# Kernel tuning notes

Hardware: AMD Instinct MI355X
Metric: run time of the kernel (lower is better)

Reference implementation:

```python
import jax, jax.numpy as jnp
import numpy as np

D_MODEL = 1024
N_HEADS = 16
D_HEAD = 64
SEQ = 2048
BATCH = 2
ATTN_SCALE = float(np.sqrt(D_HEAD))  # cfg.use_attn_scale = True
NEG_INF = -1e9


def setup_inputs() -> dict:
    key = jax.random.key(0)
    ks = jax.random.split(key, 8)
    s = 0.02
    return {
        "query_input": jax.random.normal(ks[0], (BATCH, SEQ, D_MODEL), jnp.float32),
        "key_input": jax.random.normal(ks[1], (BATCH, SEQ, D_MODEL), jnp.float32),
        "value_input": jax.random.normal(ks[2], (BATCH, SEQ, D_MODEL), jnp.float32),
        "W_Q": jax.random.normal(ks[3], (N_HEADS, D_MODEL, D_HEAD), jnp.float32) * s,
        "W_K": jax.random.normal(ks[4], (N_HEADS, D_MODEL, D_HEAD), jnp.float32) * s,
        "W_V": jax.random.normal(ks[5], (N_HEADS, D_MODEL, D_HEAD), jnp.float32) * s,
        "W_O": jax.random.normal(ks[6], (N_HEADS, D_HEAD, D_MODEL), jnp.float32) * s,
        "b_Q": jnp.zeros((N_HEADS, D_HEAD), jnp.float32),
        "b_K": jnp.zeros((N_HEADS, D_HEAD), jnp.float32),
        "b_V": jnp.zeros((N_HEADS, D_HEAD), jnp.float32),
        "b_O": jnp.zeros((D_MODEL,), jnp.float32),
    }


def reference(query_input, key_input, value_input, W_Q, W_K, W_V, W_O, b_Q, b_K, b_V, b_O):
    # QKV projections: [batch, pos, d_model] x [head, d_model, d_head] -> [batch, pos, head, d_head]
    q = jnp.einsum("bpd,hde->bphe", query_input, W_Q) + b_Q
    k = jnp.einsum("bpd,hde->bphe", key_input, W_K) + b_K
    v = jnp.einsum("bpd,hde->bphe", value_input, W_V) + b_V

    # attn scores [batch, head, query_pos, key_pos]
    scores = jnp.einsum("bqhe,bkhe->bhqk", q, k) / ATTN_SCALE

    # causal mask (attn_type == 'global'): tril over [n_ctx, n_ctx] sliced to seq
    causal = jnp.tril(jnp.ones((SEQ, SEQ), bool))
    scores = jnp.where(causal[None, None, :, :], scores, NEG_INF)

    pattern = jax.nn.softmax(scores, axis=-1)

    # z: [batch, query_pos, head, d_head]
    z = jnp.einsum("bhqk,bkhe->bqhe", pattern, v)

    # output projection: [batch, pos, d_model]
    out = jnp.einsum("bqhe,hed->bqd", z, W_O) + b_O
    return out
```

## Files before the change

kernel.cpp:

```cpp
#include <hip/hip_runtime.h>
#include <stdint.h>


typedef __attribute__((ext_vector_type(8))) short short8;
typedef __attribute__((ext_vector_type(4))) float floatx4;
typedef __attribute__((ext_vector_type(4))) unsigned int uintx4;

#define MFMA16(a, b, c) __builtin_amdgcn_mfma_f32_16x16x32_bf16(a, b, c, 0, 0, 0)

__device__ __forceinline__ unsigned short f2b(float f) {
  unsigned int u = __builtin_bit_cast(unsigned int, f);
  u = (u + 0x7fffu + ((u >> 16) & 1u)) >> 16;
  return (unsigned short)u;
}
__device__ __forceinline__ float exp2f_fast(float x) {
#if __has_builtin(__builtin_amdgcn_exp2f)
  return __builtin_amdgcn_exp2f(x);
#else
  return exp2f(x);
#endif
}
__device__ __forceinline__ unsigned int pack2_bf16(float lo, float hi) {
#if __has_builtin(__builtin_amdgcn_perm)
  return __builtin_amdgcn_perm(__builtin_bit_cast(unsigned int, hi),
                               __builtin_bit_cast(unsigned int, lo), 0x07060302u);
#else
  return (__builtin_bit_cast(unsigned int, lo) >> 16) |
         (__builtin_bit_cast(unsigned int, hi) & 0xffff0000u);
#endif
}

__device__ __forceinline__ void async_copy16(void* lds, const void* g) {
  __builtin_amdgcn_global_load_lds(
      (const __attribute__((address_space(1))) unsigned int*)g,
      (__attribute__((address_space(3))) unsigned int*)lds, 16, 0, 0);
}

__global__ __launch_bounds__(256) void conv_x3(const float* __restrict__ a,
                                               const float* __restrict__ b,
                                               const float* __restrict__ c,
                                               unsigned short* __restrict__ out) {
  const float* in = (blockIdx.y == 0) ? a : ((blockIdx.y == 1) ? b : c);
  size_t i = (size_t)blockIdx.x * 256 + threadIdx.x;
  float4 v = ((const float4*)in)[i];
  ushort4 u;
  u.x = f2b(v.x); u.y = f2b(v.y); u.z = f2b(v.z); u.w = f2b(v.w);
  ((ushort4*)(out + (size_t)blockIdx.y * 4194304))[i] = u;
}

__global__ __launch_bounds__(256) void conv_w3(const float* __restrict__ a,
                                               const float* __restrict__ b,
                                               const float* __restrict__ c,
                                               unsigned short* __restrict__ out) {
  __shared__ float T[64][65];
  const float* in = (blockIdx.y == 0) ? a : ((blockIdx.y == 1) ? b : c);
  const int t = threadIdx.x, rr = t >> 4, cc = t & 15;
  const int h = blockIdx.x >> 4, d0 = (blockIdx.x & 15) << 6;
#pragma unroll
  for (int it = 0; it < 4; ++it) {
    int dl = it * 16 + rr;
    float4 v = *(const float4*)&in[(size_t)h * 65536 + (size_t)(d0 + dl) * 64 + cc * 4];
    T[dl][cc * 4 + 0] = v.x; T[dl][cc * 4 + 1] = v.y;
    T[dl][cc * 4 + 2] = v.z; T[dl][cc * 4 + 3] = v.w;
  }
  __syncthreads();
  unsigned short* ob = out + (size_t)blockIdx.y * 1048576;
#pragma unroll
  for (int it = 0; it < 4; ++it) {
    int e = it * 16 + rr;
    ushort4 u;
    u.x = f2b(T[cc * 4 + 0][e]); u.y = f2b(T[cc * 4 + 1][e]);
    u.z = f2b(T[cc * 4 + 2][e]); u.w = f2b(T[cc * 4 + 3][e]);
    *(ushort4*)&ob[(size_t)(h * 64 + e) * 1024 + d0 + cc * 4] = u;
  }
}

__global__ __launch_bounds__(256) void conv_wo(const float* __restrict__ in,
                                               unsigned short* __restrict__ out) {
  __shared__ float T[64][65];
  const int t = threadIdx.x, rr = t >> 4, cc = t & 15;
  const int r0 = (blockIdx.x & 15) << 6;
  const int c0 = (blockIdx.x >> 4) << 6;
#pragma unroll
  for (int it = 0; it < 4; ++it) {
    int rl = it * 16 + rr;
    float4 v = *(const float4*)&in[(size_t)(r0 + rl) * 1024 + c0 + cc * 4];
    T[rl][cc * 4 + 0] = v.x; T[rl][cc * 4 + 1] = v.y;
    T[rl][cc * 4 + 2] = v.z; T[rl][cc * 4 + 3] = v.w;
  }
  __syncthreads();
#pragma unroll
  for (int it = 0; it < 4; ++it) {
    int dl = it * 16 + rr;
    ushort4 u;
    u.x = f2b(T[cc * 4 + 0][dl]); u.y = f2b(T[cc * 4 + 1][dl]);
    u.z = f2b(T[cc * 4 + 2][dl]); u.w = f2b(T[cc * 4 + 3][dl]);
    *(ushort4*)&out[(size_t)(c0 + dl) * 1024 + r0 + cc * 4] = u;
  }
}

__global__ __launch_bounds__(256) void gemm_qkvo(
    const short* __restrict__ A, const short* __restrict__ Bt,
    const float* __restrict__ bias, unsigned short* __restrict__ outb,
    float* __restrict__ outf, int mode, float scale) {
  __shared__ short As[64 * 32];
  __shared__ short Bs[64 * 32];

  const int tid = threadIdx.x;
  const int lane = tid & 63, w = tid >> 6;
  const int quad = lane >> 4, col = lane & 15;
  const int m0 = blockIdx.y * 64, n0 = blockIdx.x * 64;

  floatx4 acc00 = {0.f, 0.f, 0.f, 0.f}, acc01 = {0.f, 0.f, 0.f, 0.f};
  floatx4 acc10 = {0.f, 0.f, 0.f, 0.f}, acc11 = {0.f, 0.f, 0.f, 0.f};
  const int lr0 = (w >> 1) * 32, lc0 = (w & 1) * 32;

  const int lr = lane >> 2, gc = (lane & 3) ^ ((lane >> 3) & 3);
  const short* ga = A + (size_t)(m0 + w * 16 + lr) * 1024 + gc * 8;
  const short* gb = Bt + (size_t)(n0 + w * 16 + lr) * 1024 + gc * 8;
  short* la = &As[w * 512];
  short* lb = &Bs[w * 512];
  const int asw = (col >> 1) & 3;

  for (int k0 = 0; k0 < 1024; k0 += 32) {
    async_copy16(la, ga + k0);
    async_copy16(lb, gb + k0);
    __syncthreads();
    short8 a0 = *(const short8*)&As[(lr0 + col) * 32 + (quad ^ asw) * 8];
    short8 a1 = *(const short8*)&As[(lr0 + 16 + col) * 32 + (quad ^ asw) * 8];
    short8 b0 = *(const short8*)&Bs[(lc0 + col) * 32 + (quad ^ asw) * 8];
    short8 b1 = *(const short8*)&Bs[(lc0 + 16 + col) * 32 + (quad ^ asw) * 8];
    acc00 = MFMA16(a0, b0, acc00);
    acc01 = MFMA16(a0, b1, acc01);
    acc10 = MFMA16(a1, b0, acc10);
    acc11 = MFMA16(a1, b1, acc11);
    __syncthreads();
  }

  floatx4 acc[2][2] = {{acc00, acc01}, {acc10, acc11}};
  const int mb = m0 + lr0, nb = n0 + lc0;
#pragma unroll
  for (int i = 0; i < 2; ++i)
#pragma unroll
    for (int j = 0; j < 2; ++j)
#pragma unroll
      for (int r = 0; r < 4; ++r) {
        int m = mb + i * 16 + quad * 4 + r;
        int n = nb + j * 16 + col;
        float v = acc[i][j][r] + bias[n];
        if (mode == 0) {
          outf[(size_t)m * 1024 + n] = v;
        } else {
          v *= scale;
          unsigned short hv = f2b(v);
          int bb = m >> 11, s = m & 2047, h = n >> 6, e = n & 63;
          size_t addr;
          if (mode == 1)
            addr = (((size_t)bb * 16 + h) * 2048 + s) * 64 + e;
          else
            addr = (((size_t)bb * 16 + h) * 64 + e) * 2048 + s;
          outb[addr] = hv;
        }
      }
}

__global__ __launch_bounds__(256) void attn(const short* __restrict__ q,
                                            const short* __restrict__ k,
                                            const short* __restrict__ vt,
                                            unsigned short* __restrict__ z) {
  __shared__ short Ks[64 * 64];
  __shared__ short Vs[64 * 64];

  const int tid = threadIdx.x;
  const int lane = tid & 63, w = tid >> 6;
  const int quad = lane >> 4, col = lane & 15;
  const int qt = 31 - (blockIdx.x >> 5), bh = blockIdx.x & 31;
  const int q0 = qt * 64, qw0 = q0 + w * 16;
  const size_t base = (size_t)bh * (2048 * 64);

  const short* qp = q + base + (size_t)(qw0 + col) * 64 + quad * 8;
  short8 bq0 = *(const short8*)qp;
  short8 bq1 = *(const short8*)(qp + 32);

  floatx4 o[4] = {{0.f,0.f,0.f,0.f},{0.f,0.f,0.f,0.f},{0.f,0.f,0.f,0.f},{0.f,0.f,0.f,0.f}};
  float m_run = -1e30f, l_run = 0.f;

  const short* kg = k + base;
  const short* vg = vt + base;
  const int ksw = col & 7;
  const int slr = lane >> 3, slc = lane & 7;
  const int sgc = slc ^ slr;
  const int srcA = ((quad & 1) << 5) + col, srcB = srcA + 16;
  const bool hiq = (quad & 2) != 0;

  for (int t = 0; t <= qt; ++t) {
    const int kv0 = t * 64;
    {
      const short* kr = kg + (size_t)(kv0 + w * 16 + slr) * 64 + sgc * 8;
      async_copy16(&Ks[(w * 16) * 64], kr);
      async_copy16(&Ks[(w * 16 + 8) * 64], kr + 8 * 64);
      const short* vr = vg + (size_t)(w * 16 + slr) * 2048 + kv0 + sgc * 8;
      async_copy16(&Vs[(w * 16) * 64], vr);
      async_copy16(&Vs[(w * 16 + 8) * 64], vr + 8 * 2048);
    }
    __syncthreads();

    const bool diag = (t == qt);
    const int mtmax = diag ? w : 3;

    floatx4 st[4];
#pragma unroll
    for (int mt = 0; mt < 4; ++mt) {
      if (mt <= mtmax) {
        const short* kb = &Ks[(mt * 16 + col) * 64];
        short8 ka0 = *(const short8*)(kb + (quad ^ ksw) * 8);
        short8 ka1 = *(const short8*)(kb + ((quad + 4) ^ ksw) * 8);
        floatx4 a = {0.f, 0.f, 0.f, 0.f};
        a = MFMA16(ka0, bq0, a);
        a = MFMA16(ka1, bq1, a);
        if (diag && mt == mtmax) {
#pragma unroll
          for (int r = 0; r < 4; ++r)
            if (quad * 4 + r > col) a[r] = -1e9f;
        }
        st[mt] = a;
      }
    }

    float pmax = -1e30f;
#pragma unroll
    for (int mt = 0; mt < 4; ++mt)
      if (mt <= mtmax) {
#pragma unroll
        for (int r = 0; r < 4; ++r) pmax = fmaxf(pmax, st[mt][r]);
      }
    pmax = fmaxf(pmax, __shfl_xor(pmax, 16, 64));
    pmax = fmaxf(pmax, __shfl_xor(pmax, 32, 64));
    float mnew = fmaxf(m_run, pmax);
    float alpha = exp2f_fast(m_run - mnew);
    m_run = mnew;

    unsigned int u01[4], u23[4];
    float lsum = 0.f;
#pragma unroll
    for (int mt = 0; mt < 4; ++mt) {
      if (mt <= mtmax) {
        float p0 = exp2f_fast(st[mt][0] - mnew);
        float p1 = exp2f_fast(st[mt][1] - mnew);
        float p2 = exp2f_fast(st[mt][2] - mnew);
        float p3 = exp2f_fast(st[mt][3] - mnew);
        lsum += (p0 + p1) + (p2 + p3);
        u01[mt] = pack2_bf16(p0, p1);
        u23[mt] = pack2_bf16(p2, p3);
      } else {
        u01[mt] = 0u; u23[mt] = 0u;
      }
    }
    lsum += __shfl_xor(lsum, 16, 64);
    lsum += __shfl_xor(lsum, 32, 64);
    l_run = l_run * alpha + lsum;

    unsigned int xA0 = (unsigned int)__shfl((int)u01[0], srcA, 64);
    unsigned int xA1 = (unsigned int)__shfl((int)u01[1], srcA, 64);
    unsigned int yA0 = (unsigned int)__shfl((int)u23[0], srcA, 64);
    unsigned int yA1 = (unsigned int)__shfl((int)u23[1], srcA, 64);
    unsigned int xB0 = (unsigned int)__shfl((int)u01[0], srcB, 64);
    unsigned int xB1 = (unsigned int)__shfl((int)u01[1], srcB, 64);
    unsigned int yB0 = (unsigned int)__shfl((int)u23[0], srcB, 64);
    unsigned int yB1 = (unsigned int)__shfl((int)u23[1], srcB, 64);
    uintx4 v0;
    v0.x = hiq ? xA1 : xA0; v0.y = hiq ? yA1 : yA0;
    v0.z = hiq ? xB1 : xB0; v0.w = hiq ? yB1 : yB0;
    short8 pf0 = __builtin_bit_cast(short8, v0);
    xA0 = (unsigned int)__shfl((int)u01[2], srcA, 64);
    xA1 = (unsigned int)__shfl((int)u01[3], srcA, 64);
    yA0 = (unsigned int)__shfl((int)u23[2], srcA, 64);
    yA1 = (unsigned int)__shfl((int)u23[3], srcA, 64);
    xB0 = (unsigned int)__shfl((int)u01[2], srcB, 64);
    xB1 = (unsigned int)__shfl((int)u01[3], srcB, 64);
    yB0 = (unsigned int)__shfl((int)u23[2], srcB, 64);
    yB1 = (unsigned int)__shfl((int)u23[3], srcB, 64);
    uintx4 v1;
    v1.x = hiq ? xA1 : xA0; v1.y = hiq ? yA1 : yA0;
    v1.z = hiq ? xB1 : xB0; v1.w = hiq ? yB1 : yB0;
    short8 pf1 = __builtin_bit_cast(short8, v1);

#pragma unroll
    for (int et = 0; et < 4; ++et) {
      const short* vb = &Vs[(et * 16 + col) * 64];
      short8 va0 = *(const short8*)(vb + (quad ^ ksw) * 8);
      short8 va1 = *(const short8*)(vb + ((quad + 4) ^ ksw) * 8);
      floatx4 t0 = o[et];
#pragma unroll
      for (int r = 0; r < 4; ++r) t0[r] *= alpha;
      t0 = MFMA16(va0, pf0, t0);
      t0 = MFMA16(va1, pf1, t0);
      o[et] = t0;
    }
    __syncthreads();
  }

  const int b = bh >> 4, h = bh & 15;
#if __has_builtin(__builtin_amdgcn_rcpf)
  const float invl = __builtin_amdgcn_rcpf(l_run);
#else
  const float invl = 1.f / l_run;
#endif
  unsigned short* zr = z + (((size_t)b * 2048 + qw0 + col) * 16 + h) * 64;
#pragma unroll
  for (int et = 0; et < 4; ++et) {
    ushort4 u;
    u.x = f2b(o[et][0] * invl); u.y = f2b(o[et][1] * invl);
    u.z = f2b(o[et][2] * invl); u.w = f2b(o[et][3] * invl);
    *(ushort4*)&zr[et * 16 + quad * 4] = u;
  }
}

extern "C" void kernel_launch(void* const* d_in, const int* in_sizes, int n_in,
                              void* d_out, int out_size, void* d_ws, size_t ws_size,
                              hipStream_t stream) {
  (void)in_sizes; (void)n_in; (void)out_size; (void)ws_size;
  const float* Xq = (const float*)d_in[0];
  const float* Xk = (const float*)d_in[1];
  const float* Xv = (const float*)d_in[2];
  const float* WQ = (const float*)d_in[3];
  const float* WK = (const float*)d_in[4];
  const float* WV = (const float*)d_in[5];
  const float* WO = (const float*)d_in[6];
  const float* bQ = (const float*)d_in[7];
  const float* bK = (const float*)d_in[8];
  const float* bV = (const float*)d_in[9];
  const float* bO = (const float*)d_in[10];
  float* out = (float*)d_out;

  unsigned short* xqb = (unsigned short*)d_ws;
  unsigned short* xkb = xqb + 4194304;
  unsigned short* xvb = xkb + 4194304;
  unsigned short* wqt = xvb + 4194304;
  unsigned short* wkt = wqt + 1048576;
  unsigned short* wvt = wkt + 1048576;
  unsigned short* wot = wvt + 1048576;
  unsigned short* qb = wot + 1048576;
  unsigned short* kb = qb + 4194304;
  unsigned short* vtb = kb + 4194304;
  unsigned short* zb = vtb + 4194304;

  conv_x3<<<dim3(4096, 3), 256, 0, stream>>>(Xq, Xk, Xv, xqb);
  conv_w3<<<dim3(256, 3), 256, 0, stream>>>(WQ, WK, WV, wqt);
  conv_wo<<<256, 256, 0, stream>>>(WO, wot);

  dim3 gg(16, 64);
  const float qscale = 0.125f * 1.44269504088896f;
  gemm_qkvo<<<gg, 256, 0, stream>>>((const short*)xqb, (const short*)wqt, bQ,
                                    qb, nullptr, 1, qscale);
  gemm_qkvo<<<gg, 256, 0, stream>>>((const short*)xkb, (const short*)wkt, bK,
                                    kb, nullptr, 1, 1.0f);
  gemm_qkvo<<<gg, 256, 0, stream>>>((const short*)xvb, (const short*)wvt, bV,
                                    vtb, nullptr, 2, 1.0f);
  attn<<<1024, 256, 0, stream>>>((const short*)qb, (const short*)kb,
                                 (const short*)vtb, zb);
  gemm_qkvo<<<gg, 256, 0, stream>>>((const short*)zb, (const short*)wot, bO,
                                    nullptr, out, 0, 1.0f);
}
```

Baseline: 248.0 us.

## Use 128x128 GEMM tiles, batch QKV projections, and widen attention query tiles

The projection GEMM moves from 64x64 to 128x128 block tiles with a 4x4 MFMA grid per wave, so each loaded fragment is reused more often. The Q, K and V projections now run as one launch using blockIdx.z instead of three. The attention kernel handles 128 query rows per block (32 per wave, in two halves), so each staged K/V tile serves twice as many queries, and the causal mask is generalized to match. The trade-offs are more registers per thread and fewer blocks: 768/256 for the GEMMs and 512 for attention, which may reduce occupancy or leave the load imbalanced.

```diff
diff --git a/kernel.cpp b/kernel.cpp
--- a/kernel.cpp
+++ b/kernel.cpp
@@ -99,55 +99,76 @@
   }
 }
 
-__global__ __launch_bounds__(256) void gemm_qkvo(
-    const short* __restrict__ A, const short* __restrict__ Bt,
-    const float* __restrict__ bias, unsigned short* __restrict__ outb,
-    float* __restrict__ outf, int mode, float scale) {
-  __shared__ short As[64 * 32];
-  __shared__ short Bs[64 * 32];
+__global__ __launch_bounds__(256) void gemm128(
+    const short* __restrict__ A0, const short* __restrict__ A1,
+    const short* __restrict__ A2, const short* __restrict__ B0,
+    const short* __restrict__ B1, const short* __restrict__ B2,
+    const float* __restrict__ bias0, const float* __restrict__ bias1,
+    const float* __restrict__ bias2, unsigned short* __restrict__ ob0,
+    unsigned short* __restrict__ ob1, unsigned short* __restrict__ ob2,
+    float* __restrict__ outf, int qkv, float qscale) {
+  __shared__ short As[128 * 32];
+  __shared__ short Bs[128 * 32];
+
+  const int z = blockIdx.z;
+  const short* A = (z == 0) ? A0 : (z == 1) ? A1 : A2;
+  const short* Bt = (z == 0) ? B0 : (z == 1) ? B1 : B2;
 
   const int tid = threadIdx.x;
   const int lane = tid & 63, w = tid >> 6;
   const int quad = lane >> 4, col = lane & 15;
-  const int m0 = blockIdx.y * 64, n0 = blockIdx.x * 64;
-
-  floatx4 acc00 = {0.f, 0.f, 0.f, 0.f}, acc01 = {0.f, 0.f, 0.f, 0.f};
-  floatx4 acc10 = {0.f, 0.f, 0.f, 0.f}, acc11 = {0.f, 0.f, 0.f, 0.f};
-  const int lr0 = (w >> 1) * 32, lc0 = (w & 1) * 32;
+  const int m0 = blockIdx.y * 128, n0 = blockIdx.x * 128;
+  const int wm = (w >> 1) * 64, wn = (w & 1) * 64;
+
+  floatx4 acc[4][4] = {};
 
   const int lr = lane >> 2, gc = (lane & 3) ^ ((lane >> 3) & 3);
-  const short* ga = A + (size_t)(m0 + w * 16 + lr) * 1024 + gc * 8;
-  const short* gb = Bt + (size_t)(n0 + w * 16 + lr) * 1024 + gc * 8;
-  short* la = &As[w * 512];
-  short* lb = &Bs[w * 512];
+  const short* ga = A + (size_t)(m0 + w * 32 + lr) * 1024 + gc * 8;
+  const short* gb = Bt + (size_t)(n0 + w * 32 + lr) * 1024 + gc * 8;
+  short* la = &As[(w * 32) * 32];
+  short* lb = &Bs[(w * 32) * 32];
   const int asw = (col >> 1) & 3;
 
   for (int k0 = 0; k0 < 1024; k0 += 32) {
-    async_copy16(la, ga + k0);
-    async_copy16(lb, gb + k0);
+    async_copy16(la, ga);
+    async_copy16(la + 16 * 32, ga + 16 * 1024);
+    async_copy16(lb, gb);
+    async_copy16(lb + 16 * 32, gb + 16 * 1024);
+    ga += 32; gb += 32;
     __syncthreads();
-    short8 a0 = *(const short8*)&As[(lr0 + col) * 32 + (quad ^ asw) * 8];
-    short8 a1 = *(const short8*)&As[(lr0 + 16 + col) * 32 + (quad ^ asw) * 8];
-    short8 b0 = *(const short8*)&Bs[(lc0 + col) * 32 + (quad ^ asw) * 8];
-    short8 b1 = *(const short8*)&Bs[(lc0 + 16 + col) * 32 + (quad ^ asw) * 8];
-    acc00 = MFMA16(a0, b0, acc00);
-    acc01 = MFMA16(a0, b1, acc01);
-    acc10 = MFMA16(a1, b0, acc10);
-    acc11 = MFMA16(a1, b1, acc11);
+    short8 af[4], bf[4];
+#pragma unroll
+    for (int mi = 0; mi < 4; ++mi)
+      af[mi] = *(const short8*)&As[(wm + mi * 16 + col) * 32 + ((quad ^ asw) * 8)];
+#pragma unroll
+    for (int nj = 0; nj < 4; ++nj)
+      bf[nj] = *(const short8*)&Bs[(wn + nj * 16 + col) * 32 + ((quad ^ asw) * 8)];
+#pragma unroll
+    for (int mi = 0; mi < 4; ++mi)
+#pragma unroll
+      for (int nj = 0; nj < 4; ++nj)
+        acc[mi][nj] = MFMA16(af[mi], bf[nj], acc[mi][nj]);
     __syncthreads();
   }
 
-  floatx4 acc[2][2] = {{acc00, acc01}, {acc10, acc11}};
-  const int mb = m0 + lr0, nb = n0 + lc0;
-#pragma unroll
-  for (int i = 0; i < 2; ++i)
-#pragma unroll
-    for (int j = 0; j < 2; ++j)
+  const float* bias = (z == 0) ? bias0 : (z == 1) ? bias1 : bias2;
+  unsigned short* outb = (z == 0) ? ob0 : (z == 1) ? ob1 : ob2;
+  const int mode = qkv ? ((z == 2) ? 2 : 1) : 0;
+  const float scale = (qkv && z == 0) ? qscale : 1.0f;
+
+  float bv[4];
+#pragma unroll
+  for (int nj = 0; nj < 4; ++nj) bv[nj] = bias[n0 + wn + nj * 16 + col];
+
+#pragma unroll
+  for (int mi = 0; mi < 4; ++mi)
+#pragma unroll
+    for (int nj = 0; nj < 4; ++nj)
 #pragma unroll
       for (int r = 0; r < 4; ++r) {
-        int m = mb + i * 16 + quad * 4 + r;
-        int n = nb + j * 16 + col;
-        float v = acc[i][j][r] + bias[n];
+        int m = m0 + wm + mi * 16 + quad * 4 + r;
+        int n = n0 + wn + nj * 16 + col;
+        float v = acc[mi][nj][r] + bv[nj];
         if (mode == 0) {
           outf[(size_t)m * 1024 + n] = v;
         } else {
@@ -164,6 +185,36 @@
       }
 }
 
+__device__ __forceinline__ void exchange4(const unsigned int* u01,
+                                          const unsigned int* u23, int srcA,
+                                          int srcB, bool hiq, short8& pf0,
+                                          short8& pf1) {
+  unsigned int xA0 = (unsigned int)__shfl((int)u01[0], srcA, 64);
+  unsigned int xA1 = (unsigned int)__shfl((int)u01[1], srcA, 64);
+  unsigned int yA0 = (unsigned int)__shfl((int)u23[0], srcA, 64);
+  unsigned int yA1 = (unsigned int)__shfl((int)u23[1], srcA, 64);
+  unsigned int xB0 = (unsigned int)__shfl((int)u01[0], srcB, 64);
+  unsigned int xB1 = (unsigned int)__shfl((int)u01[1], srcB, 64);
+  unsigned int yB0 = (unsigned int)__shfl((int)u23[0], srcB, 64);
+  unsigned int yB1 = (unsigned int)__shfl((int)u23[1], srcB, 64);
+  uintx4 v0;
+  v0.x = hiq ? xA1 : xA0; v0.y = hiq ? yA1 : yA0;
+  v0.z = hiq ? xB1 : xB0; v0.w = hiq ? yB1 : yB0;
+  pf0 = __builtin_bit_cast(short8, v0);
+  xA0 = (unsigned int)__shfl((int)u01[2], srcA, 64);
+  xA1 = (unsigned int)__shfl((int)u01[3], srcA, 64);
+  yA0 = (unsigned int)__shfl((int)u23[2], srcA, 64);
+  yA1 = (unsigned int)__shfl((int)u23[3], srcA, 64);
+  xB0 = (unsigned int)__shfl((int)u01[2], srcB, 64);
+  xB1 = (unsigned int)__shfl((int)u01[3], srcB, 64);
+  yB0 = (unsigned int)__shfl((int)u23[2], srcB, 64);
+  yB1 = (unsigned int)__shfl((int)u23[3], srcB, 64);
+  uintx4 v1;
+  v1.x = hiq ? xA1 : xA0; v1.y = hiq ? yA1 : yA0;
+  v1.z = hiq ? xB1 : xB0; v1.w = hiq ? yB1 : yB0;
+  pf1 = __builtin_bit_cast(short8, v1);
+}
+
 __global__ __launch_bounds__(256) void attn(const short* __restrict__ q,
                                             const short* __restrict__ k,
                                             const short* __restrict__ vt,
@@ -174,26 +225,31 @@
   const int tid = threadIdx.x;
   const int lane = tid & 63, w = tid >> 6;
   const int quad = lane >> 4, col = lane & 15;
-  const int qt = 31 - (blockIdx.x >> 5), bh = blockIdx.x & 31;
-  const int q0 = qt * 64, qw0 = q0 + w * 16;
+  const int qt = 15 - (blockIdx.x >> 5), bh = blockIdx.x & 31;
+  const int q0 = qt * 128, qw0 = q0 + w * 32;
   const size_t base = (size_t)bh * (2048 * 64);
 
-  const short* qp = q + base + (size_t)(qw0 + col) * 64 + quad * 8;
-  short8 bq0 = *(const short8*)qp;
-  short8 bq1 = *(const short8*)(qp + 32);
-
-  floatx4 o[4] = {{0.f,0.f,0.f,0.f},{0.f,0.f,0.f,0.f},{0.f,0.f,0.f,0.f},{0.f,0.f,0.f,0.f}};
-  float m_run = -1e30f, l_run = 0.f;
+  short8 bq[2][2];
+#pragma unroll
+  for (int h = 0; h < 2; ++h) {
+    const short* qp = q + base + (size_t)(qw0 + h * 16 + col) * 64 + quad * 8;
+    bq[h][0] = *(const short8*)qp;
+    bq[h][1] = *(const short8*)(qp + 32);
+  }
+
+  floatx4 o[2][4] = {};
+  float m_run[2] = {-1e30f, -1e30f}, l_run[2] = {0.f, 0.f};
 
   const short* kg = k + base;
   const short* vg = vt + base;
   const int ksw = col & 7;
-  const int slr = lane >> 3, slc = lane & 7;
-  const int sgc = slc ^ slr;
+  const int slr = lane >> 3, sgc = (lane & 7) ^ slr;
   const int srcA = ((quad & 1) << 5) + col, srcB = srcA + 16;
   const bool hiq = (quad & 2) != 0;
-
-  for (int t = 0; t <= qt; ++t) {
+  const int qlw = w * 32 + col;
+  const int ntiles = 2 * qt + 2;
+
+  for (int t = 0; t < ntiles; ++t) {
     const int kv0 = t * 64;
     {
       const short* kr = kg + (size_t)(kv0 + w * 16 + slr) * 64 + sgc * 8;
@@ -205,114 +261,114 @@
     }
     __syncthreads();
 
-    const bool diag = (t == qt);
-    const int mtmax = diag ? w : 3;
-
-    floatx4 st[4];
-#pragma unroll
-    for (int mt = 0; mt < 4; ++mt) {
-      if (mt <= mtmax) {
-        const short* kb = &Ks[(mt * 16 + col) * 64];
-        short8 ka0 = *(const short8*)(kb + (quad ^ ksw) * 8);
-        short8 ka1 = *(const short8*)(kb + ((quad + 4) ^ ksw) * 8);
-        floatx4 a = {0.f, 0.f, 0.f, 0.f};
-        a = MFMA16(ka0, bq0, a);
-        a = MFMA16(ka1, bq1, a);
-        if (diag && mt == mtmax) {
-#pragma unroll
-          for (int r = 0; r < 4; ++r)
-            if (quad * 4 + r > col) a[r] = -1e9f;
+    const int dbase = kv0 - q0;
+    const bool diag = (dbase >= 0);
+    const int mtneed = diag ? ((32 * w + 31 - dbase) >> 4) : 3;
+
+    if (mtneed >= 0) {
+      const int mmax = (mtneed > 3) ? 3 : mtneed;
+
+      floatx4 st[2][4];
+#pragma unroll
+      for (int mt = 0; mt < 4; ++mt) {
+        if (mt <= mmax) {
+          const short* kb = &Ks[(mt * 16 + col) * 64];
+          short8 ka0 = *(const short8*)(kb + (quad ^ ksw) * 8);
+          short8 ka1 = *(const short8*)(kb + ((quad + 4) ^ ksw) * 8);
+#pragma unroll
+          for (int h = 0; h < 2; ++h) {
+            floatx4 a = {0.f, 0.f, 0.f, 0.f};
+            a = MFMA16(ka0, bq[h][0], a);
+            a = MFMA16(ka1, bq[h][1], a);
+            if (diag) {
+              const int kl = dbase + mt * 16 + quad * 4;
+              const int ql = qlw + h * 16;
+#pragma unroll
+              for (int r = 0; r < 4; ++r)
+                if (kl + r > ql) a[r] = -1e9f;
+            }
+            st[h][mt] = a;
+          }
         }
-        st[mt] = a;
+      }
+
+      float alpha[2];
+      unsigned int u01[2][4], u23[2][4];
+#pragma unroll
+      for (int h = 0; h < 2; ++h) {
+        float pmax = -3e38f;
+#pragma unroll
+        for (int mt = 0; mt < 4; ++mt)
+          if (mt <= mmax) {
+#pragma unroll
+            for (int r = 0; r < 4; ++r) pmax = fmaxf(pmax, st[h][mt][r]);
+          }
+        pmax = fmaxf(pmax, __shfl_xor(pmax, 16, 64));
+        pmax = fmaxf(pmax, __shfl_xor(pmax, 32, 64));
+        float mnew = fmaxf(m_run[h], pmax);
+        alpha[h] = exp2f_fast(m_run[h] - mnew);
+        m_run[h] = mnew;
+        float lsum = 0.f;
+#pragma unroll
+        for (int mt = 0; mt < 4; ++mt) {
+          if (mt <= mmax) {
+            float p0 = exp2f_fast(st[h][mt][0] - mnew);
+            float p1 = exp2f_fast(st[h][mt][1] - mnew);
+            float p2 = exp2f_fast(st[h][mt][2] - mnew);
+            float p3 = exp2f_fast(st[h][mt][3] - mnew);
+            lsum += (p0 + p1) + (p2 + p3);
+            u01[h][mt] = pack2_bf16(p0, p1);
+            u23[h][mt] = pack2_bf16(p2, p3);
+          } else {
+            u01[h][mt] = 0u; u23[h][mt] = 0u;
+          }
+        }
+        lsum += __shfl_xor(lsum, 16, 64);
+        lsum += __shfl_xor(lsum, 32, 64);
+        l_run[h] = l_run[h] * alpha[h] + lsum;
+      }
+
+      short8 pf0[2], pf1[2];
+#pragma unroll
+      for (int h = 0; h < 2; ++h)
+        exchange4(u01[h], u23[h], srcA, srcB, hiq, pf0[h], pf1[h]);
+
+#pragma unroll
+      for (int et = 0; et < 4; ++et) {
+        const short* vb = &Vs[(et * 16 + col) * 64];
+        short8 va0 = *(const short8*)(vb + (quad ^ ksw) * 8);
+        short8 va1 = *(const short8*)(vb + ((quad + 4) ^ ksw) * 8);
+#pragma unroll
+        for (int h = 0; h < 2; ++h) {
+          floatx4 t0 = o[h][et];
+#pragma unroll
+          for (int r = 0; r < 4; ++r) t0[r] *= alpha[h];
+          t0 = MFMA16(va0, pf0[h], t0);
+          t0 = MFMA16(va1, pf1[h], t0);
+          o[h][et] = t0;
+        }
       }
     }
-
-    float pmax = -1e30f;
-#pragma unroll
-    for (int mt = 0; mt < 4; ++mt)
-      if (mt <= mtmax) {
-#pragma unroll
-        for (int r = 0; r < 4; ++r) pmax = fmaxf(pmax, st[mt][r]);
-      }
-    pmax = fmaxf(pmax, __shfl_xor(pmax, 16, 64));
-    pmax = fmaxf(pmax, __shfl_xor(pmax, 32, 64));
-    float mnew = fmaxf(m_run, pmax);
-    float alpha = exp2f_fast(m_run - mnew);
-    m_run = mnew;
-
-    unsigned int u01[4], u23[4];
-    float lsum = 0.f;
-#pragma unroll
-    for (int mt = 0; mt < 4; ++mt) {
-      if (mt <= mtmax) {
-        float p0 = exp2f_fast(st[mt][0] - mnew);
-        float p1 = exp2f_fast(st[mt][1] - mnew);
-        float p2 = exp2f_fast(st[mt][2] - mnew);
-        float p3 = exp2f_fast(st[mt][3] - mnew);
-        lsum += (p0 + p1) + (p2 + p3);
-        u01[mt] = pack2_bf16(p0, p1);
-        u23[mt] = pack2_bf16(p2, p3);
-      } else {
-        u01[mt] = 0u; u23[mt] = 0u;
-      }
+    __syncthreads();
+  }
+
+  const int bb = bh >> 4, hh = bh & 15;
+#pragma unroll
+  for (int h = 0; h < 2; ++h) {
+#if __has_builtin(__builtin_amdgcn_rcpf)
+    const float invl = __builtin_amdgcn_rcpf(l_run[h]);
+#else
+    const float invl = 1.f / l_run[h];
+#endif
+    unsigned short* zr =
+        z + (((size_t)bb * 2048 + qw0 + h * 16 + col) * 16 + hh) * 64;
+#pragma unroll
+    for (int et = 0; et < 4; ++et) {
+      ushort4 u;
+      u.x = f2b(o[h][et][0] * invl); u.y = f2b(o[h][et][1] * invl);
+      u.z = f2b(o[h][et][2] * invl); u.w = f2b(o[h][et][3] * invl);
+      *(ushort4*)&zr[et * 16 + quad * 4] = u;
     }
-    lsum += __shfl_xor(lsum, 16, 64);
-    lsum += __shfl_xor(lsum, 32, 64);
-    l_run = l_run * alpha + lsum;
-
-    unsigned int xA0 = (unsigned int)__shfl((int)u01[0], srcA, 64);
-    unsigned int xA1 = (unsigned int)__shfl((int)u01[1], srcA, 64);
-    unsigned int yA0 = (unsigned int)__shfl((int)u23[0], srcA, 64);
-    unsigned int yA1 = (unsigned int)__shfl((int)u23[1], srcA, 64);
-    unsigned int xB0 = (unsigned int)__shfl((int)u01[0], srcB, 64);
-    unsigned int xB1 = (unsigned int)__shfl((int)u01[1], srcB, 64);
-    unsigned int yB0 = (unsigned int)__shfl((int)u23[0], srcB, 64);
-    unsigned int yB1 = (unsigned int)__shfl((int)u23[1], srcB, 64);
-    uintx4 v0;
-    v0.x = hiq ? xA1 : xA0; v0.y = hiq ? yA1 : yA0;
-    v0.z = hiq ? xB1 : xB0; v0.w = hiq ? yB1 : yB0;
-    short8 pf0 = __builtin_bit_cast(short8, v0);
-    xA0 = (unsigned int)__shfl((int)u01[2], srcA, 64);
-    xA1 = (unsigned int)__shfl((int)u01[3], srcA, 64);
-    yA0 = (unsigned int)__shfl((int)u23[2], srcA, 64);
-    yA1 = (unsigned int)__shfl((int)u23[3], srcA, 64);
-    xB0 = (unsigned int)__shfl((int)u01[2], srcB, 64);
-    xB1 = (unsigned int)__shfl((int)u01[3], srcB, 64);
-    yB0 = (unsigned int)__shfl((int)u23[2], srcB, 64);
-    yB1 = (unsigned int)__shfl((int)u23[3], srcB, 64);
-    uintx4 v1;
-    v1.x = hiq ? xA1 : xA0; v1.y = hiq ? yA1 : yA0;
-    v1.z = hiq ? xB1 : xB0; v1.w = hiq ? yB1 : yB0;
-    short8 pf1 = __builtin_bit_cast(short8, v1);
-
-#pragma unroll
-    for (int et = 0; et < 4; ++et) {
-      const short* vb = &Vs[(et * 16 + col) * 64];
-      short8 va0 = *(const short8*)(vb + (quad ^ ksw) * 8);
-      short8 va1 = *(const short8*)(vb + ((quad + 4) ^ ksw) * 8);
-      floatx4 t0 = o[et];
-#pragma unroll
-      for (int r = 0; r < 4; ++r) t0[r] *= alpha;
-      t0 = MFMA16(va0, pf0, t0);
-      t0 = MFMA16(va1, pf1, t0);
-      o[et] = t0;
-    }
-    __syncthreads();
-  }
-
-  const int b = bh >> 4, h = bh & 15;
-#if __has_builtin(__builtin_amdgcn_rcpf)
-  const float invl = __builtin_amdgcn_rcpf(l_run);
-#else
-  const float invl = 1.f / l_run;
-#endif
-  unsigned short* zr = z + (((size_t)b * 2048 + qw0 + col) * 16 + h) * 64;
-#pragma unroll
-  for (int et = 0; et < 4; ++et) {
-    ushort4 u;
-    u.x = f2b(o[et][0] * invl); u.y = f2b(o[et][1] * invl);
-    u.z = f2b(o[et][2] * invl); u.w = f2b(o[et][3] * invl);
-    *(ushort4*)&zr[et * 16 + quad * 4] = u;
   }
 }
 
@@ -349,16 +405,17 @@
   conv_w3<<<dim3(256, 3), 256, 0, stream>>>(WQ, WK, WV, wqt);
   conv_wo<<<256, 256, 0, stream>>>(WO, wot);
 
-  dim3 gg(16, 64);
   const float qscale = 0.125f * 1.44269504088896f;
-  gemm_qkvo<<<gg, 256, 0, stream>>>((const short*)xqb, (const short*)wqt, bQ,
-                                    qb, nullptr, 1, qscale);
-  gemm_qkvo<<<gg, 256, 0, stream>>>((const short*)xkb, (const short*)wkt, bK,
-                                    kb, nullptr, 1, 1.0f);
-  gemm_qkvo<<<gg, 256, 0, stream>>>((const short*)xvb, (const short*)wvt, bV,
-                                    vtb, nullptr, 2, 1.0f);
-  attn<<<1024, 256, 0, stream>>>((const short*)qb, (const short*)kb,
-                                 (const short*)vtb, zb);
-  gemm_qkvo<<<gg, 256, 0, stream>>>((const short*)zb, (const short*)wot, bO,
-                                    nullptr, out, 0, 1.0f);
-}
+  gemm128<<<dim3(8, 32, 3), 256, 0, stream>>>(
+      (const short*)xqb, (const short*)xkb, (const short*)xvb,
+      (const short*)wqt, (const short*)wkt, (const short*)wvt, bQ, bK, bV, qb,
+      kb, vtb, nullptr, 1, qscale);
+
+  attn<<<512, 256, 0, stream>>>((const short*)qb, (const short*)kb,
+                                (const short*)vtb, zb);
+
+  gemm128<<<dim3(8, 32, 1), 256, 0, stream>>>(
+      (const short*)zb, (const short*)zb, (const short*)zb, (const short*)wot,
+      (const short*)wot, (const short*)wot, bO, bO, bO, nullptr, nullptr,
+      nullptr, out, 0, 1.0f);
+}
```

Measured after the change: 258.3 us. +4.1%, slower.
